# Optimization experiments

Measured on AMD Instinct MI355X. Metric: run time of the kernel, lower is better.

The kernel has to match this reference:

```python
import jax, jax.numpy as jnp
import numpy as np

H = 3072; NH = 24; HD = 128; MLP_D = 12288
B = 1; IMG = 1536; REF = 512; TXT = 256

def _gelu_tanh(x):
    return jax.nn.gelu(x, approximate=True)

def _ln(x, eps=1e-6):
    m = jnp.mean(x, axis=-1, keepdims=True)
    v = jnp.var(x, axis=-1, keepdims=True)
    return (x - m) * jax.lax.rsqrt(v + eps)

def _rms(x, g, eps=1e-6):
    return x * jax.lax.rsqrt(jnp.mean(x * x, axis=-1, keepdims=True) + eps) * g

def _rot_half(x):
    # interleaved rotate-half: (x0,x1,x2,x3,...) -> (-x1,x0,-x3,x2,...)
    x2 = x.reshape(x.shape[:-1] + (-1, 2))
    return jnp.stack([-x2[..., 1], x2[..., 0]], axis=-1).reshape(x.shape)

def setup_inputs():
    key = jax.random.key(0)
    ks = jax.random.split(key, 16)
    s = 0.02
    # rope tables for image tokens (interleaved layout, values repeated x2)
    inv_freq = 1.0 / (10000.0 ** (jnp.arange(0, HD // 2, dtype=jnp.float32) / (HD // 2)))
    ang = jnp.arange(IMG, dtype=jnp.float32)[:, None] * inv_freq[None, :]   # [IMG, HD//2]
    ang = jnp.repeat(ang, 2, axis=-1)                                       # [IMG, HD]
    return {
        'x':   jax.random.normal(ks[0], (B, IMG + TXT, H), jnp.float32),
        'vec': jax.random.normal(ks[1], (B, H), jnp.float32),
        'ref': jax.random.normal(ks[2], (B, REF, H), jnp.float32),
        'cos': jnp.cos(ang), 'sin': jnp.sin(ang),
        'mod_w':  jax.random.normal(ks[3], (H, 3 * H), jnp.float32) * s,
        'mod_b':  jnp.zeros((3 * H,), jnp.float32),
        'rf1_w':  jax.random.normal(ks[4], (H, H), jnp.float32) * s,
        'rf1_b':  jnp.zeros((H,), jnp.float32),
        'rf2_w':  jax.random.normal(ks[5], (H, H), jnp.float32) * s,
        'rf2_b':  jnp.zeros((H,), jnp.float32),
        'rln_g':  jnp.ones((H,), jnp.float32),
        'rln_b':  jnp.zeros((H,), jnp.float32),
        'lin1_w': jax.random.normal(ks[6], (H, 3 * H + MLP_D), jnp.float32) * s,
        'lin1_b': jnp.zeros((3 * H + MLP_D,), jnp.float32),
        'q_g':    jnp.ones((HD,), jnp.float32),
        'k_g':    jnp.ones((HD,), jnp.float32),
        'lin2_w': jax.random.normal(ks[7], (H + MLP_D, H), jnp.float32) * s,
        'lin2_b': jnp.zeros((H,), jnp.float32),
        'text_mask': jnp.ones((B, TXT), jnp.int32),
        'img_len': IMG, 'txt_len': TXT,
    }

def _forward(x, vec, ref, cos, sin, mod_w, mod_b, rf1_w, rf1_b, rf2_w, rf2_b,
             rln_g, rln_b, lin1_w, lin1_b, q_g, k_g, lin2_w, lin2_b,
             text_mask, img_len, txt_len):
    Bb = x.shape[0]
    ref_len = ref.shape[1]
    # modulation (ModulateDiT: SiLU -> Linear -> chunk(3))
    mod = jnp.dot(jax.nn.silu(vec), mod_w) + mod_b
    shift, scale, gate = jnp.split(mod, 3, axis=-1)
    x_mod = _ln(x) * (1.0 + scale[:, None]) + shift[:, None]
    # ref MLP + affine LayerNorm
    r = jnp.dot(_gelu_tanh(jnp.dot(ref, rf1_w) + rf1_b), rf2_w) + rf2_b
    r = _ln(r) * rln_g + rln_b
    # token reassembly: [img | ref | txt]
    xc = jnp.concatenate([x_mod[:, :img_len], r, x_mod[:, img_len:]], axis=1)
    h = jnp.dot(xc, lin1_w) + lin1_b
    qkv, mlp = h[..., :3 * H], h[..., 3 * H:]
    L2 = xc.shape[1]
    q, k, v = [t.reshape(Bb, L2, NH, HD) for t in jnp.split(qkv, 3, axis=-1)]
    # q drops the ref span; ref contributes K/V only
    q = jnp.concatenate([q[:, :img_len], q[:, img_len + ref_len:]], axis=1)
    q = _rms(q, q_g)
    k = _rms(k, k_g)
    # rotary only on image tokens
    c = cos[None, :, None, :]; s = sin[None, :, None, :]
    img_q = q[:, :img_len] * c + _rot_half(q[:, :img_len]) * s
    img_k = k[:, :img_len] * c + _rot_half(k[:, :img_len]) * s
    q = jnp.concatenate([img_q, q[:, img_len:]], axis=1)          # [B, Lq, NH, HD]
    k = jnp.concatenate([img_k, k[:, img_len:]], axis=1)          # [B, Lkv, NH, HD]
    # varlen mask (cu_seqlens semantics): valid attends valid, pad attends pad
    tmask = text_mask.astype(bool)
    qv  = jnp.concatenate([jnp.ones((Bb, img_len), bool), tmask], axis=1)
    kvv = jnp.concatenate([jnp.ones((Bb, img_len + ref_len), bool), tmask], axis=1)
    allowed = (qv[:, None, :, None] == kvv[:, None, None, :])     # [B,1,Lq,Lkv]
    scores = jnp.einsum('bqhd,bkhd->bhqk', q, k) * (HD ** -0.5)
    scores = jnp.where(allowed, scores, jnp.asarray(-1e9, scores.dtype))
    p = jax.nn.softmax(scores, axis=-1)
    attn = jnp.einsum('bhqk,bkhd->bqhd', p, v).reshape(Bb, img_len + txt_len, H)
    mlp = jnp.concatenate([mlp[:, :img_len], mlp[:, img_len + ref_len:]], axis=1)
    out = jnp.dot(jnp.concatenate([attn, _gelu_tanh(mlp)], axis=-1), lin2_w) + lin2_b
    return x + out * gate[:, None]

def reference(x, vec, ref, cos, sin, mod_w, mod_b, rf1_w, rf1_b, rf2_w, rf2_b,
              rln_g, rln_b, lin1_w, lin1_b, q_g, k_g, lin2_w, lin2_b,
              text_mask, img_len, txt_len):
    return _forward(x, vec, ref, cos, sin, mod_w, mod_b, rf1_w, rf1_b, rf2_w, rf2_b,
                    rln_g, rln_b, lin1_w, lin1_b, q_g, k_g, lin2_w, lin2_b,
                    text_mask, img_len, txt_len)
```

## Files before the change

kernel.cpp:

```cpp
#include <hip/hip_runtime.h>
#include <cstdint>
#include <cstddef>

typedef unsigned short u16;
typedef unsigned int   u32;
typedef __bf16 bf16_t;
typedef bf16_t bf16x8 __attribute__((ext_vector_type(8)));
typedef float  f32x4  __attribute__((ext_vector_type(4)));
typedef u16    u16x4  __attribute__((ext_vector_type(4)));


__device__ __forceinline__ float b2f(u16 b){ u32 u=((u32)b)<<16; float f; __builtin_memcpy(&f,&u,4); return f; }
__device__ __forceinline__ u16 f2b(float f){ u32 u; __builtin_memcpy(&u,&f,4); u = u + 0x7fffu + ((u>>16)&1u); return (u16)(u>>16); }
__device__ __forceinline__ float gelu_f(float x){
  const float u2 = 1.5957691216057308f*(x + 0.044715f*x*x*x);
  return x/(1.f + __expf(-u2));
}

__device__ __forceinline__ void gload_lds16(const void* g, void* l){
  __builtin_amdgcn_global_load_lds((const __attribute__((address_space(1))) void*)g,
                                   (__attribute__((address_space(3))) void*)l, 16, 0, 0);
}

template<int NW, bool MX>
__device__ __forceinline__ float bred(float v, float* red){
  #pragma unroll
  for (int o=32;o;o>>=1){ float u=__shfl_down(v,o,64); v = MX? fmaxf(v,u) : v+u; }
  const int t = threadIdx.x;
  if ((t&63)==0) red[t>>6]=v;
  __syncthreads();
  float r = red[0];
  #pragma unroll
  for (int i=1;i<NW;i++) r = MX? fmaxf(r,red[i]) : r+red[i];
  __syncthreads();
  return r;
}

__device__ __forceinline__ void unpack8(uint4 u, float* f){
  f[0]=b2f((u16)(u.x&0xffffu)); f[1]=b2f((u16)(u.x>>16));
  f[2]=b2f((u16)(u.y&0xffffu)); f[3]=b2f((u16)(u.y>>16));
  f[4]=b2f((u16)(u.z&0xffffu)); f[5]=b2f((u16)(u.z>>16));
  f[6]=b2f((u16)(u.w&0xffffu)); f[7]=b2f((u16)(u.w>>16));
}
__device__ __forceinline__ uint4 pack8(const float* f){
  uint4 u;
  u.x = (u32)f2b(f[0]) | ((u32)f2b(f[1])<<16);
  u.y = (u32)f2b(f[2]) | ((u32)f2b(f[3])<<16);
  u.z = (u32)f2b(f[4]) | ((u32)f2b(f[5])<<16);
  u.w = (u32)f2b(f[6]) | ((u32)f2b(f[7])<<16);
  return u;
}

__global__ void modv_part(const float* __restrict__ vec, const float* __restrict__ W,
                          float* __restrict__ part){
  __shared__ float s[128];
  const int t = threadIdx.x;
  const int j = blockIdx.x*256 + t;
  const int i0 = blockIdx.y*128;
  if (t < 128){ float v = vec[i0+t]; s[t] = v/(1.f+__expf(-v)); }
  __syncthreads();
  float acc = 0.f;
  #pragma unroll 8
  for (int i=0;i<128;i++) acc += s[i]*W[(size_t)(i0+i)*9216 + j];
  part[(size_t)blockIdx.y*9216 + j] = acc;
}
__global__ void modv_reduce(const float* __restrict__ part, const float* __restrict__ mb,
                            float* __restrict__ modp){
  const int j = blockIdx.x*256 + threadIdx.x;
  float a = mb[j];
  #pragma unroll
  for (int c=0;c<24;c++) a += part[(size_t)c*9216 + j];
  modp[j] = a;
}

__global__ __launch_bounds__(256)
void convT(const float* __restrict__ W, u16* __restrict__ Wt, int Kd, int Nd){
  __shared__ float Ls[64][65];
  const int t = threadIdx.x;
  const int n0 = blockIdx.x*64, k0 = blockIdx.y*64;
  const int tr = t>>4;
  const int tc = (t&15)*4;
  #pragma unroll
  for (int p=0;p<4;p++){
    const int kk = tr + p*16;
    const float4 v = *(const float4*)(W + (size_t)(k0+kk)*Nd + n0 + tc);
    Ls[kk][tc+0]=v.x; Ls[kk][tc+1]=v.y; Ls[kk][tc+2]=v.z; Ls[kk][tc+3]=v.w;
  }
  __syncthreads();
  #pragma unroll
  for (int p=0;p<4;p++){
    const int nn = tr + p*16;
    u16x4 o;
    o.x = f2b(Ls[tc+0][nn]); o.y = f2b(Ls[tc+1][nn]);
    o.z = f2b(Ls[tc+2][nn]); o.w = f2b(Ls[tc+3][nn]);
    *(u16x4*)(Wt + (size_t)(n0+nn)*Kd + k0 + tc) = o;
  }
}

__global__ void convertF2B(const float* __restrict__ src, u16* __restrict__ dst){
  const size_t i = ((size_t)blockIdx.x*256 + threadIdx.x)*4;
  const float4 v = *(const float4*)(src+i);
  u16x4 o; o.x=f2b(v.x); o.y=f2b(v.y); o.z=f2b(v.z); o.w=f2b(v.w);
  *(u16x4*)(dst+i) = o;
}

__global__ void ln_modulate(const float* __restrict__ x, const float* __restrict__ modp,
                            u16* __restrict__ xc){
  __shared__ float red[4];
  const int row = blockIdx.x, t = threadIdx.x;
  const float* xr = x + (size_t)row*3072;
  float4 v[3]; float s=0.f, ss=0.f;
  #pragma unroll
  for (int k=0;k<3;k++){
    v[k] = *(const float4*)(xr + t*4 + k*1024);
    s  += v[k].x+v[k].y+v[k].z+v[k].w;
    ss += v[k].x*v[k].x+v[k].y*v[k].y+v[k].z*v[k].z+v[k].w*v[k].w;
  }
  s  = bred<4,false>(s, red);
  ss = bred<4,false>(ss, red);
  const float mean = s*(1.f/3072.f);
  const float inv = rsqrtf(ss*(1.f/3072.f)-mean*mean + 1e-6f);
  const int orow = row<1536 ? row : row+512;
  u16* o = xc + (size_t)orow*3072;
  const float* shiftp = modp; const float* scalep = modp+3072;
  #pragma unroll
  for (int k=0;k<3;k++){
    const int j = t*4 + k*1024;
    const float4 sc = *(const float4*)(scalep+j);
    const float4 sh = *(const float4*)(shiftp+j);
    u16x4 ov;
    ov.x = f2b((v[k].x-mean)*inv*(1.f+sc.x)+sh.x);
    ov.y = f2b((v[k].y-mean)*inv*(1.f+sc.y)+sh.y);
    ov.z = f2b((v[k].z-mean)*inv*(1.f+sc.z)+sh.z);
    ov.w = f2b((v[k].w-mean)*inv*(1.f+sc.w)+sh.w);
    *(u16x4*)(o+j) = ov;
  }
}

__global__ void ln_ref(const float* __restrict__ rt, const float* __restrict__ g,
                       const float* __restrict__ b, u16* __restrict__ xc){
  __shared__ float red[4];
  const int row = blockIdx.x, t = threadIdx.x;
  const float* xr = rt + (size_t)row*3072;
  float4 v[3]; float s=0.f, ss=0.f;
  #pragma unroll
  for (int k=0;k<3;k++){
    v[k] = *(const float4*)(xr + t*4 + k*1024);
    s  += v[k].x+v[k].y+v[k].z+v[k].w;
    ss += v[k].x*v[k].x+v[k].y*v[k].y+v[k].z*v[k].z+v[k].w*v[k].w;
  }
  s  = bred<4,false>(s, red);
  ss = bred<4,false>(ss, red);
  const float mean = s*(1.f/3072.f);
  const float inv = rsqrtf(ss*(1.f/3072.f)-mean*mean + 1e-6f);
  u16* o = xc + (size_t)(1536+row)*3072;
  #pragma unroll
  for (int k=0;k<3;k++){
    const int j = t*4 + k*1024;
    const float4 gv = *(const float4*)(g+j);
    const float4 bv = *(const float4*)(b+j);
    u16x4 ov;
    ov.x = f2b((v[k].x-mean)*inv*gv.x+bv.x);
    ov.y = f2b((v[k].y-mean)*inv*gv.y+bv.y);
    ov.z = f2b((v[k].z-mean)*inv*gv.z+bv.z);
    ov.w = f2b((v[k].w-mean)*inv*gv.w+bv.w);
    *(u16x4*)(o+j) = ov;
  }
}

__global__ void qk_prep(const u16* __restrict__ h, const float* __restrict__ qg,
                        const float* __restrict__ kg, const float* __restrict__ cosb,
                        const float* __restrict__ sinb, u16* __restrict__ Q,
                        u16* __restrict__ Kb){
  __shared__ float red[4];
  const int row = blockIdx.x, hd = blockIdx.y, d = threadIdx.x;
  const u16* hr = h + (size_t)row*21504;
  const float kv = b2f(hr[3072 + hd*128 + d]);
  const bool doq = (row < 1536) || (row >= 2048);
  const float qv = doq ? b2f(hr[hd*128 + d]) : 0.f;
  float a = kv*kv, b = qv*qv;
  #pragma unroll
  for (int o=32;o;o>>=1){ a += __shfl_down(a,o,64); b += __shfl_down(b,o,64); }
  if ((d&63)==0){ red[(d>>6)*2] = a; red[(d>>6)*2+1] = b; }
  __syncthreads();
  const float kinv = rsqrtf((red[0]+red[2])*(1.f/128.f) + 1e-6f);
  const float qinv = rsqrtf((red[1]+red[3])*(1.f/128.f) + 1e-6f);
  float kn = kv*kinv*kg[d];
  float qn = qv*qinv*qg[d];
  if (row < 1536){
    const float c  = cosb[row*128 + d];
    const float sn = sinb[row*128 + d];
    const float ko = b2f(hr[3072 + hd*128 + (d^1)])*kinv*kg[d^1];
    const float qo = b2f(hr[hd*128 + (d^1)])*qinv*qg[d^1];
    const float krh = (d&1) ? ko : -ko;
    const float qrh = (d&1) ? qo : -qo;
    kn = kn*c + krh*sn;
    qn = qn*c + qrh*sn;
  }
  Kb[((size_t)hd*2304 + row)*128 + d] = f2b(kn);
  if (doq){
    const int qrow = row<1536 ? row : row-512;
    Q[((size_t)hd*1792 + qrow)*128 + d] = f2b(qn);
  }
}

__global__ void v_transpose(const u16* __restrict__ h, u16* __restrict__ VT){
  __shared__ u16 Ls[32][33];
  const int tx = threadIdx.x, ty = threadIdx.y;
  const int l0 = blockIdx.x*32, d0 = blockIdx.y*32, hd = blockIdx.z;
  #pragma unroll
  for (int r=0;r<4;r++)
    Ls[ty+r*8][tx] = h[(size_t)(l0+ty+r*8)*21504 + 6144 + hd*128 + d0 + tx];
  __syncthreads();
  #pragma unroll
  for (int r=0;r<4;r++)
    VT[((size_t)hd*128 + d0+ty+r*8)*2304 + l0 + tx] = Ls[tx][ty+r*8];
}

__global__ void gelu_mlp(const u16* __restrict__ h, u16* __restrict__ out2){
  const int q = blockIdx.x;
  const int hrow = q<1536 ? q : q+512;
  const int j = blockIdx.y*2048 + threadIdx.x*8;
  const uint4 u = *(const uint4*)(h + (size_t)hrow*21504 + 9216 + j);
  float f[8]; unpack8(u, f);
  #pragma unroll
  for (int e=0;e<8;e++) f[e] = gelu_f(f[e]);
  const uint4 o = pack8(f);
  *(uint4*)(out2 + (size_t)q*15360 + 3072 + j) = o;
}

template<int EPI>
__global__ __launch_bounds__(256)
void gemm_bt(const u16* __restrict__ A, const u16* __restrict__ Bt,
             const float* __restrict__ bias, void* __restrict__ Cv,
             int K, int ldA, int ldB, int ldC,
             long long sA, long long sB, long long sC)
{
  __shared__ u16 As[128*32];
  __shared__ u16 Bs[128*32];
  const int t = threadIdx.x;
  const int w = t>>6, lane = t&63;
  const int bm = blockIdx.y, bn = blockIdx.x, bz = blockIdx.z;
  const u16* Ab = A + (size_t)((long long)bz*sA) + (size_t)bm*128*ldA;
  const u16* Bb = Bt + (size_t)((long long)bz*sB) + (size_t)bn*128*ldB;
  const int wm = w>>1, wn = w&1;
  const int lr = lane&15, lk = lane>>4;
  const int row0 = t>>2, kp0 = (t&3)*8;
  char* AsB = (char*)As; char* BsB = (char*)Bs;
  const int off0 = w*1024;
  const int off1 = 4096 + w*1024;
  f32x4 acc[4][4] = {};

  for (int kt = 0; kt < K; kt += 32){
    __syncthreads();
    gload_lds16(Ab + (size_t)row0*ldA + kt + kp0,      AsB + off0);
    gload_lds16(Ab + (size_t)(row0+64)*ldA + kt + kp0, AsB + off1);
    gload_lds16(Bb + (size_t)row0*ldB + kt + kp0,      BsB + off0);
    gload_lds16(Bb + (size_t)(row0+64)*ldB + kt + kp0, BsB + off1);
    __syncthreads();
    bf16x8 av[4], bv[4];
    #pragma unroll
    for (int i=0;i<4;i++) av[i] = *(const bf16x8*)(As + (wm*64+i*16+lr)*32 + lk*8);
    #pragma unroll
    for (int j=0;j<4;j++) bv[j] = *(const bf16x8*)(Bs + (wn*64+j*16+lr)*32 + lk*8);
    #pragma unroll
    for (int i=0;i<4;i++)
      #pragma unroll
      for (int j=0;j<4;j++)
        acc[i][j] = __builtin_amdgcn_mfma_f32_16x16x32_bf16(av[i], bv[j], acc[i][j], 0,0,0);
  }

  const int mBase = bm*128 + wm*64;
  const int nBase = bn*128 + wn*64;
  #pragma unroll
  for (int i=0;i<4;i++){
    #pragma unroll
    for (int j=0;j<4;j++){
      #pragma unroll
      for (int r=0;r<4;r++){
        const int m = mBase + i*16 + lk*4 + r;
        const int n = nBase + j*16 + lr;
        const float v = acc[i][j][r];
        const long long idx = (long long)bz*sC + (long long)m*ldC + n;
        if (EPI==6){
          ((float*)Cv)[idx] = v;
        } else {
          ((u16*)Cv)[idx] = f2b(v + bias[n]);
        }
      }
    }
  }
}

__global__ void comb_gelu(const float* __restrict__ P, const float* __restrict__ b,
                          u16* __restrict__ o){
  const size_t e = ((size_t)blockIdx.x*256 + threadIdx.x)*4;
  const int n = (int)(e % 3072);
  const size_t S = (size_t)512*3072;
  float4 a = *(const float4*)(P + e);
  #pragma unroll
  for (int c=1;c<6;c++){
    const float4 p = *(const float4*)(P + c*S + e);
    a.x+=p.x; a.y+=p.y; a.z+=p.z; a.w+=p.w;
  }
  const float4 bb = *(const float4*)(b + n);
  u16x4 ov;
  ov.x = f2b(gelu_f(a.x+bb.x)); ov.y = f2b(gelu_f(a.y+bb.y));
  ov.z = f2b(gelu_f(a.z+bb.z)); ov.w = f2b(gelu_f(a.w+bb.w));
  *(u16x4*)(o + e) = ov;
}
__global__ void comb_bias(const float* __restrict__ P, const float* __restrict__ b,
                          float* __restrict__ o){
  const size_t e = ((size_t)blockIdx.x*256 + threadIdx.x)*4;
  const int n = (int)(e % 3072);
  const size_t S = (size_t)512*3072;
  float4 a = *(const float4*)(P + e);
  #pragma unroll
  for (int c=1;c<6;c++){
    const float4 p = *(const float4*)(P + c*S + e);
    a.x+=p.x; a.y+=p.y; a.z+=p.z; a.w+=p.w;
  }
  const float4 bb = *(const float4*)(b + n);
  float4 ov; ov.x=a.x+bb.x; ov.y=a.y+bb.y; ov.z=a.z+bb.z; ov.w=a.w+bb.w;
  *(float4*)(o + e) = ov;
}

#define G256_BAR()  __builtin_amdgcn_s_barrier()
#define G256_LGKM() do{ asm volatile("s_waitcnt lgkmcnt(0)" ::: "memory"); \
                        __builtin_amdgcn_sched_barrier(0); }while(0)
#define G256_VM4()  asm volatile("s_waitcnt vmcnt(4)" ::: "memory")
#define G256_VM0()  asm volatile("s_waitcnt vmcnt(0)" ::: "memory")

__device__ __forceinline__ void lin1_map(int tw, int& bm, int& bn){
  if (tw < 504){
    const int band = tw/252; const int rr = tw - band*252;
    bn = rr/3; bm = band*3 + (rr - bn*3);
  } else if (tw < 588){
    bm = 8; bn = tw - 504;
  } else {
    const int rem = tw - 588;
    bm = 6 + (rem&1); bn = 12 + (rem>>1);
  }
}

template<int CEPI>
__global__ __launch_bounds__(512,2)
void gemm256(const u16* __restrict__ A, const u16* __restrict__ Bt,
             const float* __restrict__ bias, void* __restrict__ Cv,
             int Kc, int ld, int ldC, int nbn, int ntile, long long sC, int nwg, int gm)
{
  __shared__ char smem[131072];
  const int t = threadIdx.x;
  const int wid = t>>6, lane = t&63;
  const int lr = lane&15, lk = lane>>4;
  const int wm = wid>>2, wn = wid&3;

  const int orig = blockIdx.x;
  const int q8 = nwg>>3, r8 = nwg&7;
  const int xcd = orig&7, jj = orig>>3;
  const int wg = (xcd<r8 ? xcd*(q8+1) : r8*(q8+1) + (xcd-r8)*q8) + jj;
  int sk, bm, bn;
  if (gm == -1){
    sk = 0; lin1_map(wg, bm, bn);
  } else if (gm > 0){
    const int band = wg / (gm*nbn);
    const int rr = wg - band*(gm*nbn);
    bn = rr / gm;
    bm = band*gm + (rr - bn*gm);
    sk = 0;
  } else {
    sk = wg / ntile;
    const int rem = wg - sk*ntile;
    bm = rem / nbn; bn = rem % nbn;
  }

  const u16* Agl = A  + (size_t)bm*256*ld + (size_t)sk*Kc;
  const u16* Bgl = Bt + (size_t)bn*256*ld + (size_t)sk*Kc;
  const int NT = Kc>>6;
  const int NI = NT>>1;

  const int d0 = wid*64 + lane;
  const int sr = d0>>3;
  const size_t soff = (size_t)sr*ld + (size_t)(((d0&7)^(sr&7))<<3);
  const int xsl0 = ((lk    ) ^ (lr&7))<<4;
  const int xsl1 = ((lk | 4) ^ (lr&7))<<4;

  char* s0A = smem;
  char* s0B = smem + 32768;
  char* s1A = smem + 65536;
  char* s1B = smem + 98304;

  f32x4 acc[8][4] = {};
  bf16x8 bv[4][2];

  auto STAGE = [&](const u16* g, int h, int kt, char* ldsMat){
    const u16* s0 = g + (size_t)(h*128)*ld + kt + soff;
    char* l0 = ldsMat + h*16384 + wid*1024;
    gload_lds16(s0, l0);
    gload_lds16(s0 + (size_t)64*ld, l0 + 8192);
  };

  STAGE(Agl, 0, 0, s0A);
  STAGE(Agl, 1, 0, s0A);
  STAGE(Bgl, 0, 0, s0B);
  STAGE(Bgl, 1, 0, s0B);
  STAGE(Bgl, 0, 64, s1B);
  STAGE(Bgl, 1, 64, s1B);
  G256_VM4();
  G256_BAR();

#define G256_PH(SA, Q, READB, SB, STG, TAILV)                                   \
  do{                                                                           \
    const char* ab = SA + (wm*128 + (Q)*32 + lr)*128;                           \
    bf16x8 a0 = *(const bf16x8*)(ab + xsl0);                                    \
    bf16x8 a1 = *(const bf16x8*)(ab + xsl1);                                    \
    bf16x8 a2 = *(const bf16x8*)(ab + 2048 + xsl0);                             \
    bf16x8 a3 = *(const bf16x8*)(ab + 2048 + xsl1);                             \
    if (READB){                                                                 \
      _Pragma("unroll")                                                         \
      for (int j=0;j<4;j++){                                                    \
        const char* bb = SB + (wn*64 + j*16 + lr)*128;                          \
        bv[j][0] = *(const bf16x8*)(bb + xsl0);                                 \
        bv[j][1] = *(const bf16x8*)(bb + xsl1);                                 \
      }                                                                         \
    }                                                                           \
    STG;                                                                        \
    G256_BAR();                                                                 \
    G256_LGKM();                                                                \
    __builtin_amdgcn_s_setprio(1);                                              \
    _Pragma("unroll")                                                           \
    for (int j=0;j<4;j++){                                                      \
      acc[(Q)*2+0][j] = __builtin_amdgcn_mfma_f32_16x16x32_bf16(a0, bv[j][0], acc[(Q)*2+0][j], 0,0,0); \
      acc[(Q)*2+0][j] = __builtin_amdgcn_mfma_f32_16x16x32_bf16(a1, bv[j][1], acc[(Q)*2+0][j], 0,0,0); \
      acc[(Q)*2+1][j] = __builtin_amdgcn_mfma_f32_16x16x32_bf16(a2, bv[j][0], acc[(Q)*2+1][j], 0,0,0); \
      acc[(Q)*2+1][j] = __builtin_amdgcn_mfma_f32_16x16x32_bf16(a3, bv[j][1], acc[(Q)*2+1][j], 0,0,0); \
    }                                                                           \
    __builtin_amdgcn_s_setprio(0);                                              \
    TAILV;                                                                      \
    G256_BAR();                                                                 \
  }while(0)

  for (int it2 = 0; it2 < NI; ++it2){
    const int t0 = it2*2;
    const bool s2 = (t0+2) < NT, s3 = (t0+3) < NT;
    const int k1 = (t0+1)<<6, k2 = (t0+2)<<6, k3 = (t0+3)<<6;

    G256_PH(s0A, 0, 1, s0B, { STAGE(Agl,0,k1,s1A); STAGE(Agl,1,k1,s1A); }, );
    G256_PH(s0A, 1, 0, s0B, if (s2) STAGE(Bgl,0,k2,s0B), );
    G256_PH(s0A, 2, 0, s0B, if (s2) STAGE(Bgl,1,k2,s0B), );
    G256_PH(s0A, 3, 0, s0B, , if (s2) G256_VM4(); else G256_VM0(); );
    G256_PH(s1A, 0, 1, s1B, if (s2) STAGE(Agl,0,k2,s0A), );
    G256_PH(s1A, 1, 0, s1B, if (s2) STAGE(Agl,1,k2,s0A), );
    G256_PH(s1A, 2, 0, s1B, if (s3) STAGE(Bgl,0,k3,s1B), );
    G256_PH(s1A, 3, 0, s1B, if (s3) STAGE(Bgl,1,k3,s1B),
            if (s3) G256_VM4(); else G256_VM0(); );
  }
#undef G256_PH

  const int mB = bm*256 + wm*128 + lk*4;
  const int nB = bn*256 + wn*64 + lr;
  #pragma unroll
  for (int fi=0; fi<8; fi++){
    #pragma unroll
    for (int j=0; j<4; j++){
      const int n = nB + j*16;
      const float bb = (CEPI==0) ? bias[n] : 0.f;
      #pragma unroll
      for (int r=0;r<4;r++){
        const int m = mB + fi*16 + r;
        if (CEPI==0){
          ((u16*)Cv)[(size_t)m*ldC + n] = f2b(acc[fi][j][r] + bb);
        } else {
          ((float*)Cv)[(size_t)sk*sC + (size_t)m*ldC + n] = acc[fi][j][r];
        }
      }
    }
  }
}

__global__ __launch_bounds__(512,4)
void flash_attn(const u16* __restrict__ Qb, const u16* __restrict__ Kb,
                const u16* __restrict__ VT, const int* __restrict__ tmask,
                u16* __restrict__ out2)
{
  __shared__ __attribute__((aligned(16))) char smf[81920];
  char* Ks0 = smf;
  char* Vs0 = smf + 32768;
  char* Ps  = smf + 65536;
  const int t = threadIdx.x, wid = t>>6, lane = t&63;
  const int lr = lane&15, hi = lane>>4;
  const int head = blockIdx.y, qt = blockIdx.x;
  const int q0 = qt*128;
  const u16* Qg = Qb + ((size_t)head*1792 + q0)*128;
  const u16* Kg = Kb + (size_t)head*2304*128;
  const u16* Vg = VT + (size_t)head*128*2304;
  const float SCALE = 0.08838834764831845f;

  u32 kbits = 0;
  #pragma unroll
  for (int i=0;i<16;i++) kbits |= (u32)(tmask[i*16 + lr] != 0) << i;
  int fqr[4];
  #pragma unroll
  for (int r=0;r<4;r++){
    const int q = q0 + wid*16 + hi*4 + r;
    fqr[r] = (q < 1536) ? 1 : (tmask[q-1536] != 0);
  }

  #pragma unroll
  for (int c=0;c<4;c++){
    const int s = c*512 + wid*64 + lane;
    const int row = s>>4, dsl = s&15;
    gload_lds16(Qg + (size_t)row*128 + ((dsl ^ (row&7))<<3),
                Vs0 + (size_t)(c*512 + wid*64)*16);
  }
  #pragma unroll
  for (int c=0;c<2;c++){
    const int s = c*512 + wid*64 + lane;
    const int row = s>>4, dsl = s&15;
    gload_lds16(Kg + (size_t)row*128 + ((dsl ^ (row&7))<<3),
                Ks0 + (size_t)(c*512 + wid*64)*16);
  }
  asm volatile("s_waitcnt vmcnt(0)" ::: "memory");
  __syncthreads();

  bf16x8 av[4];
  {
    const int row = wid*16 + lr;
    #pragma unroll
    for (int ks=0;ks<4;ks++)
      av[ks] = *(const bf16x8*)(Vs0 + row*256 + (((ks*4+hi) ^ (row&7))<<4));
  }
  asm volatile("s_waitcnt lgkmcnt(0)" ::: "memory");
  __builtin_amdgcn_sched_barrier(0);
  __syncthreads();

  #pragma unroll
  for (int c=0;c<2;c++){
    const int s = c*512 + wid*64 + lane;
    const int row = s>>3, dsl = s&7;
    gload_lds16(Vg + (size_t)row*2304 + ((dsl ^ (row&7))<<3),
                Vs0 + (size_t)(c*512 + wid*64)*16);
  }
  asm volatile("s_waitcnt vmcnt(0)" ::: "memory");
  __syncthreads();

  f32x4 acc[8] = {};
  float m_[4], l_[4];
  #pragma unroll
  for (int r=0;r<4;r++){ m_[r] = -3e38f; l_[r] = 0.f; }

  for (int kt = 0; kt < 36; ++kt){
    char* Kc = Ks0 + (kt&1)*16384;
    char* Vc = Vs0 + (kt&1)*16384;
    if (kt+1 < 36){
      char* Kn = Ks0 + ((kt+1)&1)*16384;
      char* Vn = Vs0 + ((kt+1)&1)*16384;
      #pragma unroll
      for (int c=0;c<2;c++){
        const int s = c*512 + wid*64 + lane;
        { const int row = s>>4, dsl = s&15;
          gload_lds16(Kg + (size_t)((kt+1)*64 + row)*128 + ((dsl ^ (row&7))<<3),
                      Kn + (size_t)(c*512 + wid*64)*16); }
        { const int row = s>>3, dsl = s&7;
          gload_lds16(Vg + (size_t)row*2304 + (kt+1)*64 + ((dsl ^ (row&7))<<3),
                      Vn + (size_t)(c*512 + wid*64)*16); }
      }
    }
    f32x4 sacc[4] = {};
    #pragma unroll
    for (int ks=0;ks<4;ks++){
      #pragma unroll
      for (int j=0;j<4;j++){
        const int row = j*16 + lr;
        bf16x8 bk = *(const bf16x8*)(Kc + row*256 + (((ks*4+hi) ^ (row&7))<<4));
        sacc[j] = __builtin_amdgcn_mfma_f32_16x16x32_bf16(av[ks], bk, sacc[j], 0,0,0);
      }
    }
    int gkj[4];
    #pragma unroll
    for (int j=0;j<4;j++)
      gkj[j] = (kt < 32) ? 1 : (int)((kbits >> ((kt-32)*4 + j)) & 1u);
    float p[4][4]; bool alw[4][4];
    float mt[4] = {-3e38f,-3e38f,-3e38f,-3e38f};
    #pragma unroll
    for (int j=0;j<4;j++){
      #pragma unroll
      for (int r=0;r<4;r++){
        const float s = sacc[j][r]*SCALE;
        const bool a = (fqr[r] == gkj[j]);
        alw[j][r] = a; p[j][r] = s;
        if (a) mt[r] = fmaxf(mt[r], s);
      }
    }
    #pragma unroll
    for (int r=0;r<4;r++){
      #pragma unroll
      for (int o=1;o<16;o<<=1) mt[r] = fmaxf(mt[r], __shfl_xor(mt[r], o, 64));
      const float nm = fmaxf(m_[r], mt[r]);
      const float cr = __expf(m_[r] - nm);
      m_[r] = nm;
      l_[r] *= cr;
      #pragma unroll
      for (int jp=0;jp<8;jp++) acc[jp][r] *= cr;
    }
    float rs[4] = {0.f,0.f,0.f,0.f};
    #pragma unroll
    for (int j=0;j<4;j++){
      #pragma unroll
      for (int r=0;r<4;r++){
        const float pv = alw[j][r] ? __expf(p[j][r] - m_[r]) : 0.f;
        p[j][r] = pv; rs[r] += pv;
      }
    }
    #pragma unroll
    for (int r=0;r<4;r++){
      #pragma unroll
      for (int o=1;o<16;o<<=1) rs[r] += __shfl_xor(rs[r], o, 64);
      l_[r] += rs[r];
    }
    #pragma unroll
    for (int j=0;j<4;j++){
      #pragma unroll
      for (int r=0;r<4;r++){
        const int q = wid*16 + hi*4 + r;
        const int k = j*16 + lr;
        *(u16*)(Ps + q*128 + (((k>>3) ^ (q&7))<<4) + (k&7)*2) = f2b(p[j][r]);
      }
    }
    asm volatile("s_waitcnt lgkmcnt(0)" ::: "memory");
    __builtin_amdgcn_sched_barrier(0);
    bf16x8 pa[2];
    {
      const int row = wid*16 + lr;
      #pragma unroll
      for (int ks2=0;ks2<2;ks2++)
        pa[ks2] = *(const bf16x8*)(Ps + row*128 + (((ks2*4+hi) ^ (row&7))<<4));
    }
    #pragma unroll
    for (int ks2=0;ks2<2;ks2++){
      #pragma unroll
      for (int jp=0;jp<8;jp++){
        const int row = jp*16 + lr;
        bf16x8 bvv = *(const bf16x8*)(Vc + row*128 + (((ks2*4+hi) ^ (row&7))<<4));
        acc[jp] = __builtin_amdgcn_mfma_f32_16x16x32_bf16(pa[ks2], bvv, acc[jp], 0,0,0);
      }
    }
    asm volatile("s_waitcnt vmcnt(0)" ::: "memory");
    __syncthreads();
  }

  float inv[4];
  #pragma unroll
  for (int r=0;r<4;r++) inv[r] = 1.f/l_[r];
  #pragma unroll
  for (int jp=0;jp<8;jp++){
    #pragma unroll
    for (int r=0;r<4;r++){
      const size_t q = q0 + wid*16 + hi*4 + r;
      out2[q*15360 + head*128 + jp*16 + lr] = f2b(acc[jp][r]*inv[r]);
    }
  }
}

__global__ void lin2_fin(const float* __restrict__ P, const float* __restrict__ x,
                         const float* __restrict__ bias, const float* __restrict__ gate,
                         float* __restrict__ out){
  const size_t e = ((size_t)blockIdx.x*256 + threadIdx.x)*4;
  const int n = (int)(e % 3072);
  const size_t S = (size_t)1792*3072;
  float4 a = *(const float4*)(P + e);
  #pragma unroll
  for (int c=1;c<6;c++){
    const float4 p = *(const float4*)(P + c*S + e);
    a.x+=p.x; a.y+=p.y; a.z+=p.z; a.w+=p.w;
  }
  const float4 bb = *(const float4*)(bias + n);
  const float4 gg = *(const float4*)(gate + n);
  const float4 xv = *(const float4*)(x + e);
  float4 o;
  o.x = xv.x + (a.x+bb.x)*gg.x;
  o.y = xv.y + (a.y+bb.y)*gg.y;
  o.z = xv.z + (a.z+bb.z)*gg.z;
  o.w = xv.w + (a.w+bb.w)*gg.w;
  *(float4*)(out + e) = o;
}

extern "C" void kernel_launch(void* const* d_in, const int* in_sizes, int n_in,
                              void* d_out, int out_size, void* d_ws, size_t ws_size,
                              hipStream_t stream)
{
  (void)in_sizes; (void)n_in; (void)out_size; (void)ws_size;
  const float* x     = (const float*)d_in[0];
  const float* vec   = (const float*)d_in[1];
  const float* ref   = (const float*)d_in[2];
  const float* cosb  = (const float*)d_in[3];
  const float* sinb  = (const float*)d_in[4];
  const float* mod_w = (const float*)d_in[5];
  const float* mod_b = (const float*)d_in[6];
  const float* rf1_w = (const float*)d_in[7];
  const float* rf1_b = (const float*)d_in[8];
  const float* rf2_w = (const float*)d_in[9];
  const float* rf2_b = (const float*)d_in[10];
  const float* rln_g = (const float*)d_in[11];
  const float* rln_b = (const float*)d_in[12];
  const float* lin1_w= (const float*)d_in[13];
  const float* lin1_b= (const float*)d_in[14];
  const float* q_g   = (const float*)d_in[15];
  const float* k_g   = (const float*)d_in[16];
  const float* lin2_w= (const float*)d_in[17];
  const float* lin2_b= (const float*)d_in[18];
  const int*   tmask = (const int*)d_in[19];
  float* out = (float*)d_out;
  char* ws = (char*)d_ws;

  float* modp = (float*)(ws + 0);
  float* part = (float*)(ws + 36864);
  u16*  w2t   = (u16*)(ws + 921600);
  u16*  Qb    = (u16*)(ws + 95293440ll);
  u16*  Kb    = (u16*)(ws + 106303488ll);
  u16*  VT    = (u16*)(ws + 120459264ll);
  u16*  out2  = (u16*)(ws + 134615040ll);
  u16*  w1t   = (u16*)(ws + 189665280ll);
  u16*  xc    = (u16*)(ws + 321785856ll);
  u16*  rf1t  = (u16*)(ws + 335941632ll);
  u16*  rf2t  = (u16*)(ws + 354816000ll);
  u16*  refb  = (u16*)(ws + 373690368ll);
  u16*  tb    = (u16*)(ws + 376836096ll);
  float* rtmp = (float*)(ws + 379981824ll);
  float* rp   = (float*)(ws + 386273280ll);
  u16*  hbuf  = (u16*)(ws + 335941632ll);
  float* p2b  = (float*)(ws + 189665280ll);

  modv_part<<<dim3(36,24),256,0,stream>>>(vec, mod_w, part);
  modv_reduce<<<36,256,0,stream>>>(part, mod_b, modp);
  convT<<<dim3(48,48),  256,0,stream>>>(rf1_w, rf1t, 3072, 3072);
  convT<<<dim3(48,48),  256,0,stream>>>(rf2_w, rf2t, 3072, 3072);
  convT<<<dim3(336,48), 256,0,stream>>>(lin1_w, w1t, 3072, 21504);
  convT<<<dim3(48,240), 256,0,stream>>>(lin2_w, w2t, 15360, 3072);
  convertF2B<<<1536,256,0,stream>>>(ref, refb);
  ln_modulate<<<1792,256,0,stream>>>(x, modp, xc);
  gemm_bt<6><<<dim3(24,4,6),256,0,stream>>>(refb, rf1t, nullptr, rp, 512, 3072,3072,3072,
                                            512,512, (long long)512*3072);
  comb_gelu<<<1536,256,0,stream>>>(rp, rf1_b, tb);
  gemm_bt<6><<<dim3(24,4,6),256,0,stream>>>(tb, rf2t, nullptr, rp, 512, 3072,3072,3072,
                                            512,512, (long long)512*3072);
  comb_bias<<<1536,256,0,stream>>>(rp, rf2_b, rtmp);
  ln_ref<<<512,256,0,stream>>>(rtmp, rln_g, rln_b, xc);
  gemm256<0><<<636,512,0,stream>>>(xc, w1t, lin1_b, hbuf, 3072, 3072, 21504, 84, 636, 0, 636, -1);
  gelu_mlp<<<dim3(1792,6),256,0,stream>>>(hbuf, out2);
  qk_prep<<<dim3(2304,24),128,0,stream>>>(hbuf, q_g, k_g, cosb, sinb, Qb, Kb);
  v_transpose<<<dim3(72,4,24),dim3(32,8),0,stream>>>(hbuf, VT);
  flash_attn<<<dim3(14,24),512,0,stream>>>(Qb, Kb, VT, tmask, out2);
  gemm256<1><<<504,512,0,stream>>>(out2, w2t, nullptr, p2b, 2560, 15360, 3072, 12, 84,
                                   (long long)1792*3072, 504, 0);
  lin2_fin<<<5376,256,0,stream>>>(p2b, x, lin2_b, modp + 6144, out);
}
```

Measured before the change: 900.1 us.

## Fuse GELU into lin1 GEMM epilogue and halve lin2 split-K partitions

The lin1 GEMM epilogue now applies bias and tanh-GELU to the MLP columns and writes them as bf16 straight into the lin2 input buffer, with the image/text row remapping done in place. This removes the separate gelu_mlp kernel and its read and write of hbuf. The lin2 GEMM drops from 6 to 3 split-K chunks (Kc 2560 to 5120, 252 workgroups), so lin2_fin reduces fewer partial buffers. The cost is lower parallelism for lin2: 252 workgroups may underfill the GPU's compute units.

```diff
diff --git a/kernel.cpp b/kernel.cpp
--- a/kernel.cpp
+++ b/kernel.cpp
@@ -34,21 +34,6 @@
   for (int i=1;i<NW;i++) r = MX? fmaxf(r,red[i]) : r+red[i];
   __syncthreads();
   return r;
-}
-
-__device__ __forceinline__ void unpack8(uint4 u, float* f){
-  f[0]=b2f((u16)(u.x&0xffffu)); f[1]=b2f((u16)(u.x>>16));
-  f[2]=b2f((u16)(u.y&0xffffu)); f[3]=b2f((u16)(u.y>>16));
-  f[4]=b2f((u16)(u.z&0xffffu)); f[5]=b2f((u16)(u.z>>16));
-  f[6]=b2f((u16)(u.w&0xffffu)); f[7]=b2f((u16)(u.w>>16));
-}
-__device__ __forceinline__ uint4 pack8(const float* f){
-  uint4 u;
-  u.x = (u32)f2b(f[0]) | ((u32)f2b(f[1])<<16);
-  u.y = (u32)f2b(f[2]) | ((u32)f2b(f[3])<<16);
-  u.z = (u32)f2b(f[4]) | ((u32)f2b(f[5])<<16);
-  u.w = (u32)f2b(f[6]) | ((u32)f2b(f[7])<<16);
-  return u;
 }
 
 __global__ void modv_part(const float* __restrict__ vec, const float* __restrict__ W,
@@ -215,18 +200,6 @@
   #pragma unroll
   for (int r=0;r<4;r++)
     VT[((size_t)hd*128 + d0+ty+r*8)*2304 + l0 + tx] = Ls[tx][ty+r*8];
-}
-
-__global__ void gelu_mlp(const u16* __restrict__ h, u16* __restrict__ out2){
-  const int q = blockIdx.x;
-  const int hrow = q<1536 ? q : q+512;
-  const int j = blockIdx.y*2048 + threadIdx.x*8;
-  const uint4 u = *(const uint4*)(h + (size_t)hrow*21504 + 9216 + j);
-  float f[8]; unpack8(u, f);
-  #pragma unroll
-  for (int e=0;e<8;e++) f[e] = gelu_f(f[e]);
-  const uint4 o = pack8(f);
-  *(uint4*)(out2 + (size_t)q*15360 + 3072 + j) = o;
 }
 
 template<int EPI>
@@ -346,7 +319,7 @@
 template<int CEPI>
 __global__ __launch_bounds__(512,2)
 void gemm256(const u16* __restrict__ A, const u16* __restrict__ Bt,
-             const float* __restrict__ bias, void* __restrict__ Cv,
+             const float* __restrict__ bias, void* __restrict__ Cv, void* __restrict__ Cv2,
              int Kc, int ld, int ldC, int nbn, int ntile, long long sC, int nwg, int gm)
 {
   __shared__ char smem[131072];
@@ -459,19 +432,35 @@
 
   const int mB = bm*256 + wm*128 + lk*4;
   const int nB = bn*256 + wn*64 + lr;
-  #pragma unroll
-  for (int fi=0; fi<8; fi++){
-    #pragma unroll
-    for (int j=0; j<4; j++){
-      const int n = nB + j*16;
-      const float bb = (CEPI==0) ? bias[n] : 0.f;
-      #pragma unroll
-      for (int r=0;r<4;r++){
-        const int m = mB + fi*16 + r;
-        if (CEPI==0){
-          ((u16*)Cv)[(size_t)m*ldC + n] = f2b(acc[fi][j][r] + bb);
-        } else {
-          ((float*)Cv)[(size_t)sk*sC + (size_t)m*ldC + n] = acc[fi][j][r];
+  if (CEPI==0 && gm==-1 && bn >= 36){
+    const int mq = (bm <= 5) ? mB : (mB - 512);
+    #pragma unroll
+    for (int fi=0; fi<8; fi++){
+      #pragma unroll
+      for (int j=0; j<4; j++){
+        const int n = nB + j*16;
+        const float bb = bias[n];
+        #pragma unroll
+        for (int r=0;r<4;r++){
+          ((u16*)Cv2)[(size_t)(mq + fi*16 + r)*15360 + (n - 6144)] = f2b(gelu_f(acc[fi][j][r] + bb));
+        }
+      }
+    }
+  } else {
+    #pragma unroll
+    for (int fi=0; fi<8; fi++){
+      #pragma unroll
+      for (int j=0; j<4; j++){
+        const int n = nB + j*16;
+        const float bb = (CEPI==0) ? bias[n] : 0.f;
+        #pragma unroll
+        for (int r=0;r<4;r++){
+          const int m = mB + fi*16 + r;
+          if (CEPI==0){
+            ((u16*)Cv)[(size_t)m*ldC + n] = f2b(acc[fi][j][r] + bb);
+          } else {
+            ((float*)Cv)[(size_t)sk*sC + (size_t)m*ldC + n] = acc[fi][j][r];
+          }
         }
       }
     }
@@ -670,7 +659,7 @@
   const size_t S = (size_t)1792*3072;
   float4 a = *(const float4*)(P + e);
   #pragma unroll
-  for (int c=1;c<6;c++){
+  for (int c=1;c<3;c++){
     const float4 p = *(const float4*)(P + c*S + e);
     a.x+=p.x; a.y+=p.y; a.z+=p.z; a.w+=p.w;
   }
@@ -746,12 +735,11 @@
                                             512,512, (long long)512*3072);
   comb_bias<<<1536,256,0,stream>>>(rp, rf2_b, rtmp);
   ln_ref<<<512,256,0,stream>>>(rtmp, rln_g, rln_b, xc);
-  gemm256<0><<<636,512,0,stream>>>(xc, w1t, lin1_b, hbuf, 3072, 3072, 21504, 84, 636, 0, 636, -1);
-  gelu_mlp<<<dim3(1792,6),256,0,stream>>>(hbuf, out2);
+  gemm256<0><<<636,512,0,stream>>>(xc, w1t, lin1_b, hbuf, out2, 3072, 3072, 21504, 84, 636, 0, 636, -1);
   qk_prep<<<dim3(2304,24),128,0,stream>>>(hbuf, q_g, k_g, cosb, sinb, Qb, Kb);
   v_transpose<<<dim3(72,4,24),dim3(32,8),0,stream>>>(hbuf, VT);
   flash_attn<<<dim3(14,24),512,0,stream>>>(Qb, Kb, VT, tmask, out2);
-  gemm256<1><<<504,512,0,stream>>>(out2, w2t, nullptr, p2b, 2560, 15360, 3072, 12, 84,
-                                   (long long)1792*3072, 504, 0);
+  gemm256<1><<<252,512,0,stream>>>(out2, w2t, nullptr, p2b, nullptr, 5120, 15360, 3072, 12, 84,
+                                   (long long)1792*3072, 252, 0);
   lin2_fin<<<5376,256,0,stream>>>(p2b, x, lin2_b, modp + 6144, out);
 }
```

Result: faster. 867.1 us, median of 2 (-3.7%).
